# Performance work log

Measured on AMD Instinct MI355X. Metric: run time of the kernel, lower is better.

## Reference

```python
import jax, jax.numpy as jnp
import numpy as np

IN_F, OUT_F = 64, 32
N = IN_F * OUT_F + OUT_F  # 2080 sampled parameters (weights + bias)
B, S = 8, 2048
SCALE_INIT = 1.0 * float(np.sqrt(2.0 / (IN_F + OUT_F)))


def setup_inputs() -> dict:
    key = jax.random.key(0)
    k_x, k_eps, k_loc, k_cov = jax.random.split(key, 4)
    x = jax.random.normal(k_x, (B, S, IN_F), dtype=jnp.float32)
    eps = jax.random.normal(k_eps, (B, S, N), dtype=jnp.float32)
    loc = 0.01 * jax.random.normal(k_loc, (N,), dtype=jnp.float32)
    logvar = jnp.full((N,), float(np.log(SCALE_INIT)), dtype=jnp.float32)
    n_off = N * (N - 1) // 2
    cov_flat = 0.001 * jax.random.normal(k_cov, (n_off,), dtype=jnp.float32)
    return {"x": x, "eps": eps, "loc": loc, "logvar": logvar, "cov_flat": cov_flat}


def reference(x, eps, loc, logvar, cov_flat):
    n = loc.shape[0]
    in_f = x.shape[-1]
    out_f = n // (in_f + 1)  # n = out*(in+1)
    # flat_to_triangular (strictly lower) + make_cholesky, vectorized scatter
    rows, cols = np.tril_indices(n, -1)
    A = jnp.zeros((n, n), dtype=x.dtype).at[rows, cols].set(cov_flat)
    L = A + jnp.diag(jnp.exp(logvar * 0.5))  # off-diag from cov, diag = std
    # MultivariateNormal rsample: loc + L @ eps (per batch sample)
    W = loc + jnp.einsum('bsn,mn->bsm', eps, L)  # [B,S,N]
    b = W[..., :out_f]
    Wm = W[..., out_f:].reshape(*W.shape[:-1], in_f, out_f)  # [B,S,in,out]
    y = jnp.einsum('bsh,bshk->bsk', x, Wm) + b
    return y
```

## Files before the change

### kernel.cpp

```cpp
#include <hip/hip_runtime.h>
#include <hip/hip_bf16.h>

#define IN_F  64
#define OUT_F 32
#define NV    2080
#define NPAD  2176
#define MM    16384
#define KK    2080

typedef __attribute__((ext_vector_type(4))) float f32x4;
typedef __bf16 bf16x8 __attribute__((ext_vector_type(8)));

using gas_ptr = const __attribute__((address_space(1))) void*;
using lds_ptr = __attribute__((address_space(3))) void*;

__global__ __launch_bounds__(256) void build_L_k(const float* __restrict__ cov,
                                                 const float* __restrict__ logvar,
                                                 __hip_bfloat16* __restrict__ LB) {
    const int idx = blockIdx.x * 256 + threadIdx.x;
    const int m = idx / KK;
    const int k = idx - m * KK;
    float v = 0.0f;
    if (m < NV) {
        if (k < m)       v = cov[(size_t)(m * (m - 1) / 2) + k];
        else if (k == m) v = expf(0.5f * logvar[m]);
    }
    LB[idx] = __float2bfloat16(v);
}

__global__ __launch_bounds__(256) void cvt_bf16_k(const float4* __restrict__ in,
                                                  ushort4* __restrict__ out) {
    const size_t i = (size_t)blockIdx.x * 256 + threadIdx.x;
    float4 v = in[i];
    union { ushort4 u; __hip_bfloat16 h[4]; } o;
    o.h[0] = __float2bfloat16(v.x);
    o.h[1] = __float2bfloat16(v.y);
    o.h[2] = __float2bfloat16(v.z);
    o.h[3] = __float2bfloat16(v.w);
    out[i] = o.u;
}

__global__ __launch_bounds__(256) void gemm_zl_k(const __hip_bfloat16* __restrict__ A,
                                                 const __hip_bfloat16* __restrict__ BT,
                                                 __hip_bfloat16* __restrict__ Z) {
    __shared__ __align__(16) __hip_bfloat16 As[128 * 32];
    __shared__ __align__(16) __hip_bfloat16 Bs[128 * 32];

    const int tid  = threadIdx.x;
    const int bm   = blockIdx.x;
    const int bn   = blockIdx.y;
    const int wave = tid >> 6;
    const int lane = tid & 63;
    const int wr   = wave >> 1;
    const int wc   = wave & 1;
    const int quad = lane >> 4;
    const int r16  = lane & 15;

    const int kblocks = min(KK / 32, 4 * bn + 4);

    const __hip_bfloat16* Ag = A  + (size_t)bm * 128 * KK;
    const __hip_bfloat16* Bg = BT + (size_t)bn * 128 * KK;

    const int c0 = tid, c1 = tid + 256;
    const int ar0 = c0 >> 2, ao0 = (c0 & 3) * 8;
    const int ar1 = c1 >> 2, ao1 = (c1 & 3) * 8;

    f32x4 acc[4][4];
#pragma unroll
    for (int i = 0; i < 4; i++)
#pragma unroll
        for (int j = 0; j < 4; j++) acc[i][j] = f32x4{0.f, 0.f, 0.f, 0.f};

    for (int kb = 0; kb < kblocks; ++kb) {
        const int k0 = kb * 32;
        __builtin_amdgcn_global_load_lds((gas_ptr)(Ag + (size_t)ar0 * KK + k0 + ao0),
                                         (lds_ptr)(As + c0 * 8), 16, 0, 0);
        __builtin_amdgcn_global_load_lds((gas_ptr)(Ag + (size_t)ar1 * KK + k0 + ao1),
                                         (lds_ptr)(As + c1 * 8), 16, 0, 0);
        __builtin_amdgcn_global_load_lds((gas_ptr)(Bg + (size_t)ar0 * KK + k0 + ao0),
                                         (lds_ptr)(Bs + c0 * 8), 16, 0, 0);
        __builtin_amdgcn_global_load_lds((gas_ptr)(Bg + (size_t)ar1 * KK + k0 + ao1),
                                         (lds_ptr)(Bs + c1 * 8), 16, 0, 0);
        asm volatile("s_waitcnt vmcnt(0)" ::: "memory");
        __syncthreads();

        bf16x8 af[4], bfr[4];
#pragma unroll
        for (int i = 0; i < 4; i++)
            af[i] = *(const bf16x8*)(As + (64 * wr + 16 * i + r16) * 32 + quad * 8);
#pragma unroll
        for (int j = 0; j < 4; j++)
            bfr[j] = *(const bf16x8*)(Bs + (64 * wc + 16 * j + r16) * 32 + quad * 8);
#pragma unroll
        for (int i = 0; i < 4; i++)
#pragma unroll
            for (int j = 0; j < 4; j++)
                acc[i][j] = __builtin_amdgcn_mfma_f32_16x16x32_bf16(af[i], bfr[j], acc[i][j], 0, 0, 0);
        __syncthreads();
    }

#pragma unroll
    for (int i = 0; i < 4; i++) {
#pragma unroll
        for (int j = 0; j < 4; j++) {
            const int row0 = bm * 128 + 64 * wr + 16 * i + quad * 4;
            const int col  = bn * 128 + 64 * wc + 16 * j + r16;
#pragma unroll
            for (int r = 0; r < 4; r++)
                Z[(size_t)(row0 + r) * NPAD + col] = __float2bfloat16(acc[i][j][r]);
        }
    }
}

__global__ __launch_bounds__(256) void epilogue_k(const __hip_bfloat16* __restrict__ Z,
                                                  const float* __restrict__ x,
                                                  const float* __restrict__ loc,
                                                  float* __restrict__ y) {
    __shared__ float locs[NV];
    __shared__ float xs[8][IN_F];
    const int tid = threadIdx.x;
    const int t0  = blockIdx.x * 8;
    for (int i = tid; i < NV; i += 256) locs[i] = loc[i];
    {
        int i = tid;
        xs[i >> 6][i & 63] = x[(size_t)(t0 + (i >> 6)) * IN_F + (i & 63)];
        i += 256;
        xs[i >> 6][i & 63] = x[(size_t)(t0 + (i >> 6)) * IN_F + (i & 63)];
    }
    __syncthreads();

    const int k  = tid & 31;
    const int tl = tid >> 5;
    const size_t t = (size_t)t0 + tl;
    const __hip_bfloat16* zr = Z + t * NPAD;

    float sum = locs[k] + __bfloat162float(zr[k]);
#pragma unroll 8
    for (int h = 0; h < IN_F; ++h) {
        const int m = OUT_F + (h << 5) + k;
        sum += xs[tl][h] * (locs[m] + __bfloat162float(zr[m]));
    }
    y[t * OUT_F + k] = sum;
}

extern "C" void kernel_launch(void* const* d_in, const int* in_sizes, int n_in,
                              void* d_out, int out_size, void* d_ws, size_t ws_size,
                              hipStream_t stream) {
    const float* x      = (const float*)d_in[0];
    const float* eps    = (const float*)d_in[1];
    const float* loc    = (const float*)d_in[2];
    const float* logvar = (const float*)d_in[3];
    const float* cov    = (const float*)d_in[4];
    float* y = (float*)d_out;

    char* ws = (char*)d_ws;
    __hip_bfloat16* EpsB = (__hip_bfloat16*)ws;
    __hip_bfloat16* LB   = (__hip_bfloat16*)(ws + (size_t)MM * KK * 2);
    __hip_bfloat16* Zb   = (__hip_bfloat16*)(ws + (size_t)MM * KK * 2
                                                + (size_t)NPAD * KK * 2);

    build_L_k<<<(NPAD * KK) / 256, 256, 0, stream>>>(cov, logvar, LB);
    cvt_bf16_k<<<(MM * KK / 4) / 256, 256, 0, stream>>>((const float4*)eps, (ushort4*)EpsB);
    gemm_zl_k<<<dim3(MM / 128, NPAD / 128), 256, 0, stream>>>(EpsB, LB, Zb);
    epilogue_k<<<MM / 8, 256, 0, stream>>>(Zb, x, loc, y);
}
```

Baseline: 367.0 us.

## Double-buffer GEMM LDS tiles with XOR swizzle, reorder blocks, widen bf16 convert

The GEMM now keeps two LDS buffers per operand. It prefetches the next K-tile with global_load_lds while the MFMAs run on the current tile, and one barrier per iteration replaces the explicit vmcnt wait. LDS chunks are XOR-swizzled by row to cut bank conflicts on the fragment reads. The block column index is reversed so the heaviest triangular blocks are scheduled first. The fp32-to-bf16 conversion handles eight elements per thread and writes 16-byte stores. Removing the explicit vmcnt(0) wait relies on the barrier to make the async LDS loads visible, which could become a race.

```diff
diff --git a/kernel.cpp b/kernel.cpp
--- a/kernel.cpp
+++ b/kernel.cpp
@@ -29,26 +29,27 @@
 }
 
 __global__ __launch_bounds__(256) void cvt_bf16_k(const float4* __restrict__ in,
-                                                  ushort4* __restrict__ out) {
+                                                  uint4* __restrict__ out) {
     const size_t i = (size_t)blockIdx.x * 256 + threadIdx.x;
-    float4 v = in[i];
-    union { ushort4 u; __hip_bfloat16 h[4]; } o;
-    o.h[0] = __float2bfloat16(v.x);
-    o.h[1] = __float2bfloat16(v.y);
-    o.h[2] = __float2bfloat16(v.z);
-    o.h[3] = __float2bfloat16(v.w);
+    float4 a = in[2 * i];
+    float4 b = in[2 * i + 1];
+    union { uint4 u; __hip_bfloat16 h[8]; } o;
+    o.h[0] = __float2bfloat16(a.x); o.h[1] = __float2bfloat16(a.y);
+    o.h[2] = __float2bfloat16(a.z); o.h[3] = __float2bfloat16(a.w);
+    o.h[4] = __float2bfloat16(b.x); o.h[5] = __float2bfloat16(b.y);
+    o.h[6] = __float2bfloat16(b.z); o.h[7] = __float2bfloat16(b.w);
     out[i] = o.u;
 }
 
 __global__ __launch_bounds__(256) void gemm_zl_k(const __hip_bfloat16* __restrict__ A,
                                                  const __hip_bfloat16* __restrict__ BT,
                                                  __hip_bfloat16* __restrict__ Z) {
-    __shared__ __align__(16) __hip_bfloat16 As[128 * 32];
-    __shared__ __align__(16) __hip_bfloat16 Bs[128 * 32];
+    __shared__ __align__(16) __hip_bfloat16 As[2][128 * 32];
+    __shared__ __align__(16) __hip_bfloat16 Bs[2][128 * 32];
 
     const int tid  = threadIdx.x;
     const int bm   = blockIdx.x;
-    const int bn   = blockIdx.y;
+    const int bn   = 16 - blockIdx.y;
     const int wave = tid >> 6;
     const int lane = tid & 63;
     const int wr   = wave >> 1;
@@ -62,8 +63,10 @@
     const __hip_bfloat16* Bg = BT + (size_t)bn * 128 * KK;
 
     const int c0 = tid, c1 = tid + 256;
-    const int ar0 = c0 >> 2, ao0 = (c0 & 3) * 8;
-    const int ar1 = c1 >> 2, ao1 = (c1 & 3) * 8;
+    const int ar0 = c0 >> 2, ap0 = (c0 & 3) ^ ((ar0 >> 1) & 3);
+    const int ar1 = c1 >> 2, ap1 = (c1 & 3) ^ ((ar1 >> 1) & 3);
+    const size_t gofs0 = (size_t)ar0 * KK + ap0 * 8;
+    const size_t gofs1 = (size_t)ar1 * KK + ap1 * 8;
 
     f32x4 acc[4][4];
 #pragma unroll
@@ -71,32 +74,42 @@
 #pragma unroll
         for (int j = 0; j < 4; j++) acc[i][j] = f32x4{0.f, 0.f, 0.f, 0.f};
 
+    int aofs[4], bofs[4];
+#pragma unroll
+    for (int i = 0; i < 4; i++) {
+        const int arow = 64 * wr + 16 * i + r16;
+        aofs[i] = arow * 32 + (quad ^ ((arow >> 1) & 3)) * 8;
+        const int brow = 64 * wc + 16 * i + r16;
+        bofs[i] = brow * 32 + (quad ^ ((brow >> 1) & 3)) * 8;
+    }
+
+    __builtin_amdgcn_global_load_lds((gas_ptr)(Ag + gofs0), (lds_ptr)(&As[0][0] + c0 * 8), 16, 0, 0);
+    __builtin_amdgcn_global_load_lds((gas_ptr)(Ag + gofs1), (lds_ptr)(&As[0][0] + c1 * 8), 16, 0, 0);
+    __builtin_amdgcn_global_load_lds((gas_ptr)(Bg + gofs0), (lds_ptr)(&Bs[0][0] + c0 * 8), 16, 0, 0);
+    __builtin_amdgcn_global_load_lds((gas_ptr)(Bg + gofs1), (lds_ptr)(&Bs[0][0] + c1 * 8), 16, 0, 0);
+
     for (int kb = 0; kb < kblocks; ++kb) {
-        const int k0 = kb * 32;
-        __builtin_amdgcn_global_load_lds((gas_ptr)(Ag + (size_t)ar0 * KK + k0 + ao0),
-                                         (lds_ptr)(As + c0 * 8), 16, 0, 0);
-        __builtin_amdgcn_global_load_lds((gas_ptr)(Ag + (size_t)ar1 * KK + k0 + ao1),
-                                         (lds_ptr)(As + c1 * 8), 16, 0, 0);
-        __builtin_amdgcn_global_load_lds((gas_ptr)(Bg + (size_t)ar0 * KK + k0 + ao0),
-                                         (lds_ptr)(Bs + c0 * 8), 16, 0, 0);
-        __builtin_amdgcn_global_load_lds((gas_ptr)(Bg + (size_t)ar1 * KK + k0 + ao1),
-                                         (lds_ptr)(Bs + c1 * 8), 16, 0, 0);
-        asm volatile("s_waitcnt vmcnt(0)" ::: "memory");
+        const int cur = kb & 1;
         __syncthreads();
+
+        if (kb + 1 < kblocks) {
+            const size_t k0 = (size_t)(kb + 1) * 32;
+            __builtin_amdgcn_global_load_lds((gas_ptr)(Ag + k0 + gofs0), (lds_ptr)(&As[cur ^ 1][0] + c0 * 8), 16, 0, 0);
+            __builtin_amdgcn_global_load_lds((gas_ptr)(Ag + k0 + gofs1), (lds_ptr)(&As[cur ^ 1][0] + c1 * 8), 16, 0, 0);
+            __builtin_amdgcn_global_load_lds((gas_ptr)(Bg + k0 + gofs0), (lds_ptr)(&Bs[cur ^ 1][0] + c0 * 8), 16, 0, 0);
+            __builtin_amdgcn_global_load_lds((gas_ptr)(Bg + k0 + gofs1), (lds_ptr)(&Bs[cur ^ 1][0] + c1 * 8), 16, 0, 0);
+        }
 
         bf16x8 af[4], bfr[4];
 #pragma unroll
-        for (int i = 0; i < 4; i++)
-            af[i] = *(const bf16x8*)(As + (64 * wr + 16 * i + r16) * 32 + quad * 8);
+        for (int i = 0; i < 4; i++) af[i]  = *(const bf16x8*)(&As[cur][0] + aofs[i]);
 #pragma unroll
-        for (int j = 0; j < 4; j++)
-            bfr[j] = *(const bf16x8*)(Bs + (64 * wc + 16 * j + r16) * 32 + quad * 8);
+        for (int j = 0; j < 4; j++) bfr[j] = *(const bf16x8*)(&Bs[cur][0] + bofs[j]);
 #pragma unroll
         for (int i = 0; i < 4; i++)
 #pragma unroll
             for (int j = 0; j < 4; j++)
                 acc[i][j] = __builtin_amdgcn_mfma_f32_16x16x32_bf16(af[i], bfr[j], acc[i][j], 0, 0, 0);
-        __syncthreads();
     }
 
 #pragma unroll
@@ -160,7 +173,7 @@
                                                 + (size_t)NPAD * KK * 2);
 
     build_L_k<<<(NPAD * KK) / 256, 256, 0, stream>>>(cov, logvar, LB);
-    cvt_bf16_k<<<(MM * KK / 4) / 256, 256, 0, stream>>>((const float4*)eps, (ushort4*)EpsB);
+    cvt_bf16_k<<<(MM * KK / 8) / 256, 256, 0, stream>>>((const float4*)eps, (uint4*)EpsB);
     gemm_zl_k<<<dim3(MM / 128, NPAD / 128), 256, 0, stream>>>(EpsB, LB, Zb);
     epilogue_k<<<MM / 8, 256, 0, stream>>>(Zb, x, loc, y);
 }
```

Measured after the change: 338.2 us. 1.09x faster.
